# Optimization experiments

Measured on AMD Instinct MI355X. Metric: run time of the kernel, lower is better.

## Reference

```python
import jax, jax.numpy as jnp
import numpy as np

L, D, H, DK, DV, DFF = 6, 512, 8, 64, 64, 2048
B, S = 8, 512
EPS = 1e-5


def _pos_table(max_len, d_model):
    pos = np.arange(max_len)[:, None].astype(np.float64)
    i = np.arange(d_model)[None, :].astype(np.float64)
    t = pos / np.power(10000.0, 2.0 * i / d_model)
    t[0, :] = 0.0
    t[1:, 0::2] = np.sin(t[1:, 0::2])
    t[1:, 1::2] = np.cos(t[1:, 1::2])
    return jnp.asarray(t, dtype=jnp.float32)


def _ln(x, g, b):
    m = jnp.mean(x, axis=-1, keepdims=True)
    v = jnp.mean(jnp.square(x - m), axis=-1, keepdims=True)
    return (x - m) * jax.lax.rsqrt(v + EPS) * g + b


def setup_inputs() -> dict:
    key = jax.random.key(0)
    ks = jax.random.split(key, 12)
    s = 0.02
    return {
        "enc_inputs": jax.random.normal(ks[0], (B, S, D), jnp.float32),
        "enc_inputs_mask": jax.random.randint(ks[1], (B, S), 0, 100, dtype=jnp.int64),
        "Wq": jax.random.normal(ks[2], (L, D, H * DK), jnp.float32) * s,
        "Wk": jax.random.normal(ks[3], (L, D, H * DK), jnp.float32) * s,
        "Wv": jax.random.normal(ks[4], (L, D, H * DV), jnp.float32) * s,
        "Wo": jax.random.normal(ks[5], (L, H * DV, D), jnp.float32) * s,
        "ln1_g": jnp.ones((L, D), jnp.float32),
        "ln1_b": jnp.zeros((L, D), jnp.float32),
        "W1": jax.random.normal(ks[6], (L, D, DFF), jnp.float32) * s,
        "W2": jax.random.normal(ks[7], (L, DFF, D), jnp.float32) * s,
        "ln2_g": jnp.ones((L, D), jnp.float32),
        "ln2_b": jnp.zeros((L, D), jnp.float32),
    }


def reference(enc_inputs, enc_inputs_mask, Wq, Wk, Wv, Wo, ln1_g, ln1_b, W1, W2, ln2_g, ln2_b):
    b, s, _ = enc_inputs.shape
    x = enc_inputs + _pos_table(s, D)  # positional encoding (dropout = eval/no-op)
    # pad mask: True where key token is pad (mask id == 0); broadcast over heads & queries
    pad = (enc_inputs_mask == 0)[:, None, None, :]  # [B,1,1,S]
    inv_sqrt_dk = np.float32(1.0 / np.sqrt(DK))
    attns = []
    for l in range(L):
        residual = x
        q = (x @ Wq[l]).reshape(b, s, H, DK).transpose(0, 2, 1, 3)  # [B,H,S,DK]
        k = (x @ Wk[l]).reshape(b, s, H, DK).transpose(0, 2, 1, 3)
        v = (x @ Wv[l]).reshape(b, s, H, DV).transpose(0, 2, 1, 3)
        scores = jnp.einsum("bhqd,bhkd->bhqk", q, k) * inv_sqrt_dk
        scores = jnp.where(pad, jnp.float32(-1e9), scores)
        attn = jax.nn.softmax(scores, axis=-1)
        ctx = jnp.einsum("bhqk,bhkd->bhqd", attn, v)
        ctx = ctx.transpose(0, 2, 1, 3).reshape(b, s, H * DV)
        x = _ln(ctx @ Wo[l] + residual, ln1_g[l], ln1_b[l])
        x = _ln(jax.nn.relu(x @ W1[l]) @ W2[l] + x, ln2_g[l], ln2_b[l])
        attns.append(attn)
    return x, jnp.stack(attns)  # [B,S,D], [L,B,H,S,S]
```

## Files before the change

kernel.cpp:

```cpp
#include <hip/hip_runtime.h>

typedef __attribute__((ext_vector_type(8))) short bf16x8;
typedef __attribute__((ext_vector_type(4))) short bf16x4;
typedef __attribute__((ext_vector_type(4))) float f32x4;

__device__ __forceinline__ float b2f(ushort u) {
  union { uint u; float f; } x; x.u = ((uint)u) << 16; return x.f;
}
__device__ __forceinline__ ushort f2b(float f) {
  union { float f; uint u; } x; x.f = f;
  uint r = x.u + 0x7fffu + ((x.u >> 16) & 1u);
  return (ushort)(r >> 16);
}
__device__ __forceinline__ f32x4 mfma16(bf16x8 a, bf16x8 b, f32x4 c) {
  return __builtin_amdgcn_mfma_f32_16x16x32_bf16(a, b, c, 0, 0, 0);
}
__device__ __forceinline__ void glds16(const ushort* g, ushort* l) {
  __builtin_amdgcn_global_load_lds((const __attribute__((address_space(1))) void*)g,
                                   (__attribute__((address_space(3))) void*)l, 16, 0, 0);
}
#define VMCNT0 asm volatile("s_waitcnt vmcnt(0)" ::: "memory")

__global__ void detect_kernel(const uint* __restrict__ ln1g, const uint* __restrict__ mask,
                              int* __restrict__ flags) {
  if (threadIdx.x == 0) {
    flags[0] = (ln1g[0] == 0x3F800000u) ? 1 : 0;
    int odd0 = 1;
    for (int i = 0; i < 16; i++)
      if (mask[2 * i + 1] != 0u) odd0 = 0;
    flags[1] = odd0;
  }
}

__device__ __forceinline__ void convt_tile(const void* __restrict__ src, ushort* __restrict__ dst,
                                           int K, int N, int l, int k0, int n0, int f) {
  __shared__ ushort T[64][72];
  size_t mo = (size_t)l * K * N;
  int r = threadIdx.x >> 2, c = (threadIdx.x & 3) * 16;
  if (f) {
    const float* sp = (const float*)src + mo + (size_t)(k0 + r) * N + n0 + c;
#pragma unroll
    for (int i = 0; i < 16; i += 4) {
      float4 fv = *(const float4*)(sp + i);
      T[c + i][r] = f2b(fv.x); T[c + i + 1][r] = f2b(fv.y);
      T[c + i + 2][r] = f2b(fv.z); T[c + i + 3][r] = f2b(fv.w);
    }
  } else {
    const ushort* sp = (const ushort*)src + mo + (size_t)(k0 + r) * N + n0 + c;
    bf16x8 v0 = *(const bf16x8*)sp;
    bf16x8 v1 = *(const bf16x8*)(sp + 8);
#pragma unroll
    for (int i = 0; i < 8; i++) { T[c + i][r] = (ushort)v0[i]; T[c + 8 + i][r] = (ushort)v1[i]; }
  }
  __syncthreads();
  ushort* d = dst + mo + (size_t)(n0 + r) * K + k0 + c;
  *(bf16x8*)d = *(const bf16x8*)&T[r][c];
  *(bf16x8*)(d + 8) = *(const bf16x8*)&T[r][c + 8];
}

__global__ __launch_bounds__(256) void convt_all_kernel(
    const void* __restrict__ Wq, const void* __restrict__ Wk, const void* __restrict__ Wv,
    const void* __restrict__ Wo, const void* __restrict__ W1, const void* __restrict__ W2,
    ushort* __restrict__ tWq, ushort* __restrict__ tWk, ushort* __restrict__ tWv,
    ushort* __restrict__ tWo, ushort* __restrict__ tW1, ushort* __restrict__ tW2,
    const int* __restrict__ flags) {
  int f = flags[0];
  int id = blockIdx.x;
  if (id < 1536) {
    const void* s; ushort* d;
    if (id < 384)       { s = Wq; d = tWq; }
    else if (id < 768)  { s = Wk; d = tWk; id -= 384; }
    else if (id < 1152) { s = Wv; d = tWv; id -= 768; }
    else                { s = Wo; d = tWo; id -= 1152; }
    int l = id >> 6, rr = id & 63;
    convt_tile(s, d, 512, 512, l, (rr & 7) * 64, (rr >> 3) * 64, f);
  } else if (id < 3072) {
    int r = id - 1536;
    int l = r >> 8, rr = r & 255;
    convt_tile(W1, tW1, 512, 2048, l, (rr & 7) * 64, (rr >> 3) * 64, f);
  } else {
    int r = id - 3072;
    int l = r >> 8, rr = r & 255;
    convt_tile(W2, tW2, 2048, 512, l, (rr & 31) * 64, (rr >> 5) * 64, f);
  }
}

__global__ __launch_bounds__(256) void posadd_kernel(const void* __restrict__ enc,
                                                     float* __restrict__ x32,
                                                     ushort* __restrict__ xb,
                                                     const int* __restrict__ flags) {
  int f = flags[0];
  int idx = blockIdx.x * 256 + threadIdx.x;
  int s = idx >> 9, d = idx & 511;
  float pef = 0.f;
  if (s > 0) {
    double t = (double)s / pow(10000.0, 2.0 * (double)d / 512.0);
    pef = (float)((d & 1) ? cos(t) : sin(t));
  }
  for (int b = 0; b < 8; b++) {
    size_t o = ((size_t)(b * 512 + s)) * 512 + d;
    float ev = f ? ((const float*)enc)[o] : b2f(((const ushort*)enc)[o]);
    float xv = ev + pef;
    x32[o] = xv;
    xb[o] = f2b(xv);
  }
}

template <bool RELU, int OUTMODE>
__device__ __forceinline__ void gemm_bt_core(const ushort* __restrict__ A,
                                             const ushort* __restrict__ Bt,
                                             ushort* __restrict__ C,
                                             int M, int N, int K, int bm, int bn) {
  __shared__ ushort As[2 * 128 * 64];
  __shared__ ushort Bs[2 * 128 * 64];
  int tid = threadIdx.x;
  int wave = tid >> 6, lane = tid & 63;
  int lm = lane & 15, lq = lane >> 4;
  int wm = (wave & 1) * 64, wn = (wave >> 1) * 64;
  int m0 = bm * 128, n0 = bn * 128;
  f32x4 z = {0.f, 0.f, 0.f, 0.f};
  f32x4 acc[4][4];
#pragma unroll
  for (int mi = 0; mi < 4; mi++)
#pragma unroll
    for (int ni = 0; ni < 4; ni++) acc[mi][ni] = z;

  int sr = tid >> 3, sc = (tid & 7) * 8;
  const ushort* ap = A + (size_t)(m0 + sr) * K + sc;
  const ushort* bp = Bt + (size_t)(n0 + sr) * K + sc;
  int nt = K >> 6;

#pragma unroll
  for (int j = 0; j < 4; j++) {
    glds16(ap + (size_t)(j * 32) * K, As + tid * 8 + j * 2048);
    glds16(bp + (size_t)(j * 32) * K, Bs + tid * 8 + j * 2048);
  }
  VMCNT0;
  __builtin_amdgcn_s_barrier();
  __builtin_amdgcn_sched_barrier(0);

  for (int t = 0; t < nt; t++) {
    int cur = (t & 1) * 8192;
    if (t + 1 < nt) {
      int nxt = ((t + 1) & 1) * 8192;
      int k0 = (t + 1) << 6;
#pragma unroll
      for (int j = 0; j < 4; j++) {
        glds16(ap + (size_t)(j * 32) * K + k0, As + nxt + tid * 8 + j * 2048);
        glds16(bp + (size_t)(j * 32) * K + k0, Bs + nxt + tid * 8 + j * 2048);
      }
    }
#pragma unroll
    for (int kk = 0; kk < 64; kk += 32) {
      bf16x8 af[4], bfv[4];
#pragma unroll
      for (int mi = 0; mi < 4; mi++)
        af[mi] = *(const bf16x8*)&As[cur + (wm + mi * 16 + lm) * 64 + kk + lq * 8];
#pragma unroll
      for (int ni = 0; ni < 4; ni++)
        bfv[ni] = *(const bf16x8*)&Bs[cur + (wn + ni * 16 + lm) * 64 + kk + lq * 8];
#pragma unroll
      for (int mi = 0; mi < 4; mi++)
#pragma unroll
        for (int ni = 0; ni < 4; ni++)
          acc[mi][ni] = mfma16(af[mi], bfv[ni], acc[mi][ni]);
    }
    VMCNT0;
    __builtin_amdgcn_s_barrier();
    __builtin_amdgcn_sched_barrier(0);
  }

  if (OUTMODE == 0) {
#pragma unroll
    for (int mi = 0; mi < 4; mi++)
#pragma unroll
      for (int ni = 0; ni < 4; ni++) {
        int row = m0 + wm + mi * 16 + lq * 4;
        int col = n0 + wn + ni * 16 + lm;
#pragma unroll
        for (int r = 0; r < 4; r++) {
          float vv = acc[mi][ni][r];
          if (RELU) vv = fmaxf(vv, 0.f);
          C[(size_t)(row + r) * N + col] = f2b(vv);
        }
      }
  } else {
#pragma unroll
    for (int mi = 0; mi < 4; mi++)
#pragma unroll
      for (int ni = 0; ni < 4; ni++) {
        int row = m0 + wm + mi * 16 + lq * 4;
        int col = n0 + wn + ni * 16 + lm;
        int b = row >> 9, s = row & 511;
        bf16x4 o;
#pragma unroll
        for (int r = 0; r < 4; r++) o[r] = (short)f2b(acc[mi][ni][r]);
        *(bf16x4*)&C[((size_t)(b * 8 + (col >> 6)) * 64 + (col & 63)) * 512 + s] = o;
      }
  }
}

template <bool RELU>
__global__ __launch_bounds__(256) void gemm_bt_kernel(const ushort* __restrict__ A,
                                                      const ushort* __restrict__ Bt,
                                                      ushort* __restrict__ C, int M, int N, int K) {
  gemm_bt_core<RELU, 0>(A, Bt, C, M, N, K, blockIdx.x, blockIdx.y);
}

template <bool RELU, int OUTMODE>
__device__ __forceinline__ void gemm64_core(const ushort* __restrict__ A,
                                            const ushort* __restrict__ Bt,
                                            ushort* __restrict__ C,
                                            int M, int N, int K, int bm, int bn) {
  __shared__ ushort As[2 * 64 * 64];
  __shared__ ushort Bs[2 * 64 * 64];
  int tid = threadIdx.x;
  int wave = tid >> 6, lane = tid & 63;
  int lm = lane & 15, lq = lane >> 4;
  int wm = (wave & 1) * 32, wn = (wave >> 1) * 32;
  int m0 = bm * 64, n0 = bn * 64;
  f32x4 z = {0.f, 0.f, 0.f, 0.f};
  f32x4 acc[2][2];
#pragma unroll
  for (int mi = 0; mi < 2; mi++)
#pragma unroll
    for (int ni = 0; ni < 2; ni++) acc[mi][ni] = z;

  int sr = tid >> 3, sc = (tid & 7) * 8;
  const ushort* ap = A + (size_t)(m0 + sr) * K + sc;
  const ushort* bp = Bt + (size_t)(n0 + sr) * K + sc;
  int nt = K >> 6;

#pragma unroll
  for (int j = 0; j < 2; j++) {
    glds16(ap + (size_t)(j * 32) * K, As + tid * 8 + j * 2048);
    glds16(bp + (size_t)(j * 32) * K, Bs + tid * 8 + j * 2048);
  }
  VMCNT0;
  __builtin_amdgcn_s_barrier();
  __builtin_amdgcn_sched_barrier(0);

  for (int t = 0; t < nt; t++) {
    int cur = (t & 1) * 4096;
    if (t + 1 < nt) {
      int nxt = ((t + 1) & 1) * 4096;
      int k0 = (t + 1) << 6;
#pragma unroll
      for (int j = 0; j < 2; j++) {
        glds16(ap + (size_t)(j * 32) * K + k0, As + nxt + tid * 8 + j * 2048);
        glds16(bp + (size_t)(j * 32) * K + k0, Bs + nxt + tid * 8 + j * 2048);
      }
    }
#pragma unroll
    for (int kk = 0; kk < 64; kk += 32) {
      bf16x8 af[2], bfv[2];
#pragma unroll
      for (int mi = 0; mi < 2; mi++)
        af[mi] = *(const bf16x8*)&As[cur + (wm + mi * 16 + lm) * 64 + kk + lq * 8];
#pragma unroll
      for (int ni = 0; ni < 2; ni++)
        bfv[ni] = *(const bf16x8*)&Bs[cur + (wn + ni * 16 + lm) * 64 + kk + lq * 8];
#pragma unroll
      for (int mi = 0; mi < 2; mi++)
#pragma unroll
        for (int ni = 0; ni < 2; ni++)
          acc[mi][ni] = mfma16(af[mi], bfv[ni], acc[mi][ni]);
    }
    VMCNT0;
    __builtin_amdgcn_s_barrier();
    __builtin_amdgcn_sched_barrier(0);
  }

  if (OUTMODE == 0) {
#pragma unroll
    for (int mi = 0; mi < 2; mi++)
#pragma unroll
      for (int ni = 0; ni < 2; ni++) {
        int row = m0 + wm + mi * 16 + lq * 4;
        int col = n0 + wn + ni * 16 + lm;
#pragma unroll
        for (int r = 0; r < 4; r++) {
          float vv = acc[mi][ni][r];
          if (RELU) vv = fmaxf(vv, 0.f);
          C[(size_t)(row + r) * N + col] = f2b(vv);
        }
      }
  } else {
#pragma unroll
    for (int mi = 0; mi < 2; mi++)
#pragma unroll
      for (int ni = 0; ni < 2; ni++) {
        int row = m0 + wm + mi * 16 + lq * 4;
        int col = n0 + wn + ni * 16 + lm;
        int b = row >> 9, s = row & 511;
        bf16x4 o;
#pragma unroll
        for (int r = 0; r < 4; r++) o[r] = (short)f2b(acc[mi][ni][r]);
        *(bf16x4*)&C[((size_t)(b * 8 + (col >> 6)) * 64 + (col & 63)) * 512 + s] = o;
      }
  }
}

template <bool RELU>
__global__ __launch_bounds__(256) void gemm64_kernel(const ushort* __restrict__ A,
                                                     const ushort* __restrict__ Bt,
                                                     ushort* __restrict__ C, int M, int N, int K) {
  gemm64_core<RELU, 0>(A, Bt, C, M, N, K, blockIdx.x, blockIdx.y);
}

__global__ __launch_bounds__(256) void gemm64_qkv_kernel(const ushort* __restrict__ A,
                                                         const ushort* __restrict__ Wq,
                                                         const ushort* __restrict__ Wk,
                                                         const ushort* __restrict__ Wv,
                                                         ushort* __restrict__ q, ushort* __restrict__ k,
                                                         ushort* __restrict__ vt, int M, int N, int K) {
  if (blockIdx.z == 0)      gemm64_core<false, 0>(A, Wq, q,  M, N, K, blockIdx.x, blockIdx.y);
  else if (blockIdx.z == 1) gemm64_core<false, 0>(A, Wk, k,  M, N, K, blockIdx.x, blockIdx.y);
  else                      gemm64_core<false, 1>(A, Wv, vt, M, N, K, blockIdx.x, blockIdx.y);
}

__global__ __launch_bounds__(256) void attn_kernel(const ushort* __restrict__ qb, const ushort* __restrict__ kb,
                                                   const ushort* __restrict__ vt, const uint* __restrict__ mask,
                                                   void* __restrict__ out_base, size_t out_elem_off,
                                                   ushort* __restrict__ ctx, const int* __restrict__ flags) {
  __shared__ ushort Qs[16][72];
  __shared__ float maskf[512];
  __shared__ float redm[4][16];
  __shared__ float reds[4][16];
  __shared__ ushort Pb[16 * 512];
  int of32 = flags[0], m64 = flags[1];
  int tid = threadIdx.x, wave = tid >> 6, lane = tid & 63;
  int lm = lane & 15, lq = lane >> 4;
  int wg = blockIdx.x;
  int slot = wg >> 3;
  int bh = (wg & 7) + 8 * (slot >> 5);
  int b = bh >> 3, h = bh & 7;
  int q0 = (slot & 31) * 16;
  {
    int r = tid >> 4, c = (tid & 15) * 4;
    const ushort* src = qb + (size_t)(b * 512 + q0 + r) * 512 + h * 64 + c;
    *(bf16x4*)&Qs[r][c] = *(const bf16x4*)src;
  }
  {
#pragma unroll
    for (int i = 0; i < 2; i++) {
      int kk = tid * 2 + i;
      uint mv = mask[(size_t)(b * 512 + kk) << m64];
      maskf[kk] = (mv == 0u) ? -1e9f : 0.f;
    }
  }
  __syncthreads();
  bf16x8 a0 = *(const bf16x8*)&Qs[lm][lq * 8];
  bf16x8 a1 = *(const bf16x8*)&Qs[lm][32 + lq * 8];
  f32x4 z = {0.f, 0.f, 0.f, 0.f};
  f32x4 acc[8];
#pragma unroll
  for (int t8 = 0; t8 < 8; t8++) {
    int key = (wave * 8 + t8) * 16 + lm;
    const ushort* kp = kb + (size_t)(b * 512 + key) * 512 + h * 64;
    bf16x8 kb0 = *(const bf16x8*)(kp + lq * 8);
    bf16x8 kb1 = *(const bf16x8*)(kp + 32 + lq * 8);
    f32x4 s = mfma16(a0, kb0, z);
    s = mfma16(a1, kb1, s);
    float mf = maskf[key];
#pragma unroll
    for (int r = 0; r < 4; r++) acc[t8][r] = s[r] * 0.125f + mf;
  }
  float rmax[4];
#pragma unroll
  for (int r = 0; r < 4; r++) {
    float v = acc[0][r];
#pragma unroll
    for (int t8 = 1; t8 < 8; t8++) v = fmaxf(v, acc[t8][r]);
    v = fmaxf(v, __shfl_xor(v, 1));
    v = fmaxf(v, __shfl_xor(v, 2));
    v = fmaxf(v, __shfl_xor(v, 4));
    v = fmaxf(v, __shfl_xor(v, 8));
    rmax[r] = v;
  }
  if (lm == 0) {
#pragma unroll
    for (int r = 0; r < 4; r++) redm[wave][lq * 4 + r] = rmax[r];
  }
  __syncthreads();
#pragma unroll
  for (int r = 0; r < 4; r++) {
    int row = lq * 4 + r;
    rmax[r] = fmaxf(fmaxf(redm[0][row], redm[1][row]), fmaxf(redm[2][row], redm[3][row]));
  }
  float rsum[4];
#pragma unroll
  for (int r = 0; r < 4; r++) {
    float s = 0.f;
#pragma unroll
    for (int t8 = 0; t8 < 8; t8++) {
      float e = expf(acc[t8][r] - rmax[r]);
      acc[t8][r] = e;
      s += e;
    }
    s += __shfl_xor(s, 1);
    s += __shfl_xor(s, 2);
    s += __shfl_xor(s, 4);
    s += __shfl_xor(s, 8);
    rsum[r] = s;
  }
  if (lm == 0) {
#pragma unroll
    for (int r = 0; r < 4; r++) reds[wave][lq * 4 + r] = rsum[r];
  }
  __syncthreads();
  float rinv[4];
#pragma unroll
  for (int r = 0; r < 4; r++) {
    int row = lq * 4 + r;
    rinv[r] = 1.f / (reds[0][row] + reds[1][row] + reds[2][row] + reds[3][row]);
  }
  if (of32) {
    float* ao = (float*)out_base;
#pragma unroll
    for (int t8 = 0; t8 < 8; t8++)
#pragma unroll
      for (int r = 0; r < 4; r++) {
        int row = lq * 4 + r, key = (wave * 8 + t8) * 16 + lm;
        float pf = acc[t8][r] * rinv[r];
        Pb[(row * 512 + key) ^ ((row & 7) << 3)] = f2b(pf);
        ao[out_elem_off + ((size_t)(b * 8 + h) * 512 + q0 + row) * 512 + key] = pf;
      }
  } else {
    ushort* ao = (ushort*)out_base;
#pragma unroll
    for (int t8 = 0; t8 < 8; t8++)
#pragma unroll
      for (int r = 0; r < 4; r++) {
        int row = lq * 4 + r, key = (wave * 8 + t8) * 16 + lm;
        ushort pb = f2b(acc[t8][r] * rinv[r]);
        Pb[(row * 512 + key) ^ ((row & 7) << 3)] = pb;
        ao[out_elem_off + ((size_t)(b * 8 + h) * 512 + q0 + row) * 512 + key] = pb;
      }
  }
  __syncthreads();
  f32x4 c = z;
  int d = wave * 16 + lm;
  const ushort* vp = vt + ((size_t)bh * 64 + d) * 512;
#pragma unroll 4
  for (int ks = 0; ks < 16; ks++) {
    bf16x8 pa = *(const bf16x8*)&Pb[(lm * 512 + ks * 32 + lq * 8) ^ ((lm & 7) << 3)];
    bf16x8 bv = *(const bf16x8*)(vp + ks * 32 + lq * 8);
    c = mfma16(pa, bv, c);
  }
#pragma unroll
  for (int r = 0; r < 4; r++) {
    ctx[(size_t)(b * 512 + q0 + lq * 4 + r) * 512 + h * 64 + d] = f2b(c[r]);
  }
}

__global__ __launch_bounds__(256) void ln_kernel(const ushort* __restrict__ a, float* __restrict__ x32,
                                                 ushort* __restrict__ xb, const void* __restrict__ g,
                                                 const void* __restrict__ bb, int goff,
                                                 const int* __restrict__ flags, void* __restrict__ fout) {
  int f = flags[0];
  int row = blockIdx.x, tid = threadIdx.x;
  size_t base = (size_t)row * 512;
  float v0 = b2f(a[base + tid]) + x32[base + tid];
  float v1 = b2f(a[base + tid + 256]) + x32[base + tid + 256];
  float s1 = v0 + v1, s2 = v0 * v0 + v1 * v1;
#pragma unroll
  for (int off = 32; off > 0; off >>= 1) {
    s1 += __shfl_down(s1, off);
    s2 += __shfl_down(s2, off);
  }
  __shared__ float r1[4], r2[4];
  if ((tid & 63) == 0) { r1[tid >> 6] = s1; r2[tid >> 6] = s2; }
  __syncthreads();
  s1 = r1[0] + r1[1] + r1[2] + r1[3];
  s2 = r2[0] + r2[1] + r2[2] + r2[3];
  float m = s1 * (1.f / 512.f);
  float var = s2 * (1.f / 512.f) - m * m;
  float rs = rsqrtf(var + 1e-5f);
  float g0, g1v, b0, b1;
  if (f) {
    const float* gp = (const float*)g + goff;
    const float* bp = (const float*)bb + goff;
    g0 = gp[tid]; g1v = gp[tid + 256]; b0 = bp[tid]; b1 = bp[tid + 256];
  } else {
    const ushort* gp = (const ushort*)g + goff;
    const ushort* bp = (const ushort*)bb + goff;
    g0 = b2f(gp[tid]); g1v = b2f(gp[tid + 256]); b0 = b2f(bp[tid]); b1 = b2f(bp[tid + 256]);
  }
  float y0 = (v0 - m) * rs * g0 + b0;
  float y1 = (v1 - m) * rs * g1v + b1;
  if (fout) {
    if (f) {
      ((float*)fout)[base + tid] = y0;
      ((float*)fout)[base + tid + 256] = y1;
    } else {
      ((ushort*)fout)[base + tid] = f2b(y0);
      ((ushort*)fout)[base + tid + 256] = f2b(y1);
    }
  } else {
    x32[base + tid] = y0;        xb[base + tid] = f2b(y0);
    x32[base + tid + 256] = y1;  xb[base + tid + 256] = f2b(y1);
  }
}

extern "C" void kernel_launch(void* const* d_in, const int* in_sizes, int n_in,
                              void* d_out, int out_size, void* d_ws, size_t ws_size,
                              hipStream_t stream) {
  const void* enc  = d_in[0];
  const uint* mask = (const uint*)d_in[1];
  const void* Wq   = d_in[2];
  const void* Wk   = d_in[3];
  const void* Wv   = d_in[4];
  const void* Wo   = d_in[5];
  const void* ln1g = d_in[6];
  const void* ln1b = d_in[7];
  const void* W1   = d_in[8];
  const void* W2   = d_in[9];
  const void* ln2g = d_in[10];
  const void* ln2b = d_in[11];

  char* p = (char*)d_ws;
  int* flags  = (int*)p;      p += 256;
  ushort* tWq = (ushort*)p;   p += (size_t)1572864 * 2;
  ushort* tWk = (ushort*)p;   p += (size_t)1572864 * 2;
  ushort* tWv = (ushort*)p;   p += (size_t)1572864 * 2;
  ushort* tWo = (ushort*)p;   p += (size_t)1572864 * 2;
  ushort* tW1 = (ushort*)p;   p += (size_t)6291456 * 2;
  ushort* tW2 = (ushort*)p;   p += (size_t)6291456 * 2;
  float*  x32 = (float*)p;    p += (size_t)2097152 * 4;
  ushort* xb  = (ushort*)p;   p += (size_t)2097152 * 2;
  ushort* g2  = (ushort*)p;   p += (size_t)2097152 * 2;
  ushort* ctx = (ushort*)p;   p += (size_t)2097152 * 2;
  ushort* q   = (ushort*)p;   p += (size_t)2097152 * 2;
  ushort* k   = (ushort*)p;   p += (size_t)2097152 * 2;
  p += (size_t)2097152 * 2;
  ushort* vt  = (ushort*)p;   p += (size_t)2097152 * 2;
  ushort* g1  = q;

  detect_kernel<<<1, 64, 0, stream>>>((const uint*)ln1g, mask, flags);
  convt_all_kernel<<<4608, 256, 0, stream>>>(Wq, Wk, Wv, Wo, W1, W2,
                                             tWq, tWk, tWv, tWo, tW1, tW2, flags);
  posadd_kernel<<<1024, 256, 0, stream>>>(enc, x32, xb, flags);

  for (int l = 0; l < 6; l++) {
    gemm64_qkv_kernel<<<dim3(64, 8, 3), 256, 0, stream>>>(
        xb, tWq + (size_t)l * 262144, tWk + (size_t)l * 262144, tWv + (size_t)l * 262144,
        q, k, vt, 4096, 512, 512);
    attn_kernel<<<2048, 256, 0, stream>>>(
        q, k, vt, mask, d_out, (size_t)2097152 + (size_t)l * 16777216, ctx, flags);
    gemm64_kernel<false><<<dim3(64, 8), 256, 0, stream>>>(ctx, tWo + (size_t)l * 262144, g2, 4096, 512, 512);
    ln_kernel<<<4096, 256, 0, stream>>>(g2, x32, xb, ln1g, ln1b, l * 512, flags, nullptr);
    gemm_bt_kernel<true><<<dim3(32, 16), 256, 0, stream>>>(xb, tW1 + (size_t)l * 1048576, g1, 4096, 2048, 512);
    gemm64_kernel<false><<<dim3(64, 8), 256, 0, stream>>>(g1, tW2 + (size_t)l * 1048576, g2, 4096, 512, 2048);
    ln_kernel<<<4096, 256, 0, stream>>>(g2, x32, xb, ln2g, ln2b, l * 512, flags,
                                        l == 5 ? d_out : nullptr);
  }
}
```

Baseline: 1.240 ms.

## Split-K the FFN down-projection GEMM and reduce partials in layernorm

The W2 GEMM (K=2048) now runs as a two-way split-K kernel with 1024 workgroups instead of 512. Each split writes fp32 partials to a new workspace buffer, and the second layernorm sums the two partials before the residual add. This targets low occupancy and long serial K loops on the 256-CU device. In exchange it adds about 32 MB of extra fp32 write and read traffic per layer.

```diff
diff --git a/kernel.cpp b/kernel.cpp
--- a/kernel.cpp
+++ b/kernel.cpp
@@ -317,6 +317,86 @@
   if (blockIdx.z == 0)      gemm64_core<false, 0>(A, Wq, q,  M, N, K, blockIdx.x, blockIdx.y);
   else if (blockIdx.z == 1) gemm64_core<false, 0>(A, Wk, k,  M, N, K, blockIdx.x, blockIdx.y);
   else                      gemm64_core<false, 1>(A, Wv, vt, M, N, K, blockIdx.x, blockIdx.y);
+}
+
+__global__ __launch_bounds__(256) void gemm64sk_kernel(const ushort* __restrict__ A,
+                                                       const ushort* __restrict__ Bt,
+                                                       float* __restrict__ Cp,
+                                                       int M, int N, int K) {
+  __shared__ ushort As[2 * 64 * 64];
+  __shared__ ushort Bs[2 * 64 * 64];
+  int kh = K >> 1;
+  int sk = blockIdx.z;
+  const ushort* Ab = A + (size_t)sk * kh;
+  const ushort* Bb = Bt + (size_t)sk * kh;
+  float* C = Cp + (size_t)sk * M * N;
+  int tid = threadIdx.x;
+  int wave = tid >> 6, lane = tid & 63;
+  int lm = lane & 15, lq = lane >> 4;
+  int wm = (wave & 1) * 32, wn = (wave >> 1) * 32;
+  int m0 = blockIdx.x * 64, n0 = blockIdx.y * 64;
+  f32x4 z = {0.f, 0.f, 0.f, 0.f};
+  f32x4 acc[2][2];
+#pragma unroll
+  for (int mi = 0; mi < 2; mi++)
+#pragma unroll
+    for (int ni = 0; ni < 2; ni++) acc[mi][ni] = z;
+
+  int sr = tid >> 3, sc = (tid & 7) * 8;
+  const ushort* ap = Ab + (size_t)(m0 + sr) * K + sc;
+  const ushort* bp = Bb + (size_t)(n0 + sr) * K + sc;
+  int nt = kh >> 6;
+
+#pragma unroll
+  for (int j = 0; j < 2; j++) {
+    glds16(ap + (size_t)(j * 32) * K, As + tid * 8 + j * 2048);
+    glds16(bp + (size_t)(j * 32) * K, Bs + tid * 8 + j * 2048);
+  }
+  VMCNT0;
+  __builtin_amdgcn_s_barrier();
+  __builtin_amdgcn_sched_barrier(0);
+
+  for (int t = 0; t < nt; t++) {
+    int cur = (t & 1) * 4096;
+    if (t + 1 < nt) {
+      int nxt = ((t + 1) & 1) * 4096;
+      int k0 = (t + 1) << 6;
+#pragma unroll
+      for (int j = 0; j < 2; j++) {
+        glds16(ap + (size_t)(j * 32) * K + k0, As + nxt + tid * 8 + j * 2048);
+        glds16(bp + (size_t)(j * 32) * K + k0, Bs + nxt + tid * 8 + j * 2048);
+      }
+    }
+#pragma unroll
+    for (int kk = 0; kk < 64; kk += 32) {
+      bf16x8 af[2], bfv[2];
+#pragma unroll
+      for (int mi = 0; mi < 2; mi++)
+        af[mi] = *(const bf16x8*)&As[cur + (wm + mi * 16 + lm) * 64 + kk + lq * 8];
+#pragma unroll
+      for (int ni = 0; ni < 2; ni++)
+        bfv[ni] = *(const bf16x8*)&Bs[cur + (wn + ni * 16 + lm) * 64 + kk + lq * 8];
+#pragma unroll
+      for (int mi = 0; mi < 2; mi++)
+#pragma unroll
+        for (int ni = 0; ni < 2; ni++)
+          acc[mi][ni] = mfma16(af[mi], bfv[ni], acc[mi][ni]);
+    }
+    VMCNT0;
+    __builtin_amdgcn_s_barrier();
+    __builtin_amdgcn_sched_barrier(0);
+  }
+
+#pragma unroll
+  for (int mi = 0; mi < 2; mi++)
+#pragma unroll
+    for (int ni = 0; ni < 2; ni++) {
+      int row = m0 + wm + mi * 16 + lq * 4;
+      int col = n0 + wn + ni * 16 + lm;
+#pragma unroll
+      for (int r = 0; r < 4; r++)
+        C[(size_t)(row + r) * N + col] = acc[mi][ni][r];
+    }
 }
 
 __global__ __launch_bounds__(256) void attn_kernel(const ushort* __restrict__ qb, const ushort* __restrict__ kb,
@@ -457,12 +537,22 @@
 __global__ __launch_bounds__(256) void ln_kernel(const ushort* __restrict__ a, float* __restrict__ x32,
                                                  ushort* __restrict__ xb, const void* __restrict__ g,
                                                  const void* __restrict__ bb, int goff,
-                                                 const int* __restrict__ flags, void* __restrict__ fout) {
+                                                 const int* __restrict__ flags, void* __restrict__ fout,
+                                                 const float* __restrict__ pa0,
+                                                 const float* __restrict__ pa1) {
   int f = flags[0];
   int row = blockIdx.x, tid = threadIdx.x;
   size_t base = (size_t)row * 512;
-  float v0 = b2f(a[base + tid]) + x32[base + tid];
-  float v1 = b2f(a[base + tid + 256]) + x32[base + tid + 256];
+  float a0v, a1v;
+  if (pa0) {
+    a0v = pa0[base + tid] + pa1[base + tid];
+    a1v = pa0[base + tid + 256] + pa1[base + tid + 256];
+  } else {
+    a0v = b2f(a[base + tid]);
+    a1v = b2f(a[base + tid + 256]);
+  }
+  float v0 = a0v + x32[base + tid];
+  float v1 = a1v + x32[base + tid + 256];
   float s1 = v0 + v1, s2 = v0 * v0 + v1 * v1;
 #pragma unroll
   for (int off = 32; off > 0; off >>= 1) {
@@ -535,6 +625,7 @@
   ushort* k   = (ushort*)p;   p += (size_t)2097152 * 2;
   p += (size_t)2097152 * 2;
   ushort* vt  = (ushort*)p;   p += (size_t)2097152 * 2;
+  float* g2p  = (float*)p;    p += (size_t)2 * 2097152 * 4;
   ushort* g1  = q;
 
   detect_kernel<<<1, 64, 0, stream>>>((const uint*)ln1g, mask, flags);
@@ -549,10 +640,11 @@
     attn_kernel<<<2048, 256, 0, stream>>>(
         q, k, vt, mask, d_out, (size_t)2097152 + (size_t)l * 16777216, ctx, flags);
     gemm64_kernel<false><<<dim3(64, 8), 256, 0, stream>>>(ctx, tWo + (size_t)l * 262144, g2, 4096, 512, 512);
-    ln_kernel<<<4096, 256, 0, stream>>>(g2, x32, xb, ln1g, ln1b, l * 512, flags, nullptr);
+    ln_kernel<<<4096, 256, 0, stream>>>(g2, x32, xb, ln1g, ln1b, l * 512, flags, nullptr,
+                                        nullptr, nullptr);
     gemm_bt_kernel<true><<<dim3(32, 16), 256, 0, stream>>>(xb, tW1 + (size_t)l * 1048576, g1, 4096, 2048, 512);
-    gemm64_kernel<false><<<dim3(64, 8), 256, 0, stream>>>(g1, tW2 + (size_t)l * 1048576, g2, 4096, 512, 2048);
+    gemm64sk_kernel<<<dim3(64, 8, 2), 256, 0, stream>>>(g1, tW2 + (size_t)l * 1048576, g2p, 4096, 512, 2048);
     ln_kernel<<<4096, 256, 0, stream>>>(g2, x32, xb, ln2g, ln2b, l * 512, flags,
-                                        l == 5 ? d_out : nullptr);
-  }
-}
+                                        l == 5 ? d_out : nullptr, g2p, g2p + (size_t)2097152);
+  }
+}
```

Result: faster. 1.209 ms (-2.5%).
